# Kernel optimization log

Hardware: AMD Instinct MI355X
Metric: run time of the kernel (lower is better)

The kernel has to match this reference:

```python
import jax, jax.numpy as jnp
import numpy as np

EPS = 1e-5

def conv(x, w, b, stride, pad):
    y = jax.lax.conv_general_dilated(x, w, (stride, stride), [(pad, pad), (pad, pad)],
                                     dimension_numbers=('NCHW', 'OIHW', 'NCHW'))
    return y + b[None, :, None, None]

def inorm(x):
    # InstanceNorm2d, affine=False, eps=1e-5, biased variance over H,W
    m = x.mean(axis=(2, 3), keepdims=True)
    v = ((x - m) ** 2).mean(axis=(2, 3), keepdims=True)
    return (x - m) * jax.lax.rsqrt(v + EPS)

def setup_inputs() -> dict:
    key = jax.random.key(0)
    ks = jax.random.split(key, 24)
    B = 64
    x = jax.random.normal(ks[0], (B, 5, 256, 192), dtype=jnp.float32)
    chans = [(5, 8), (8, 16), (16, 32), (32, 64), (64, 128), (128, 256)]
    params = {'x': x}
    for i, (ci, co) in enumerate(chans):
        fan = ci * 16
        params[f'w{i}'] = jax.random.normal(ks[1 + 2 * i], (co, ci, 4, 4), jnp.float32) / np.sqrt(fan)
        params[f'b{i}'] = jnp.zeros((co,), jnp.float32)
    for i in (6, 7):
        params[f'w{i}'] = jax.random.normal(ks[1 + 2 * i], (256, 256, 3, 3), jnp.float32) / np.sqrt(256 * 9)
        params[f'b{i}'] = jnp.zeros((256,), jnp.float32)
    params['fc1_w'] = jax.random.normal(ks[20], (128, 512), jnp.float32) / np.sqrt(512)
    params['fc1_b'] = jnp.zeros((128,), jnp.float32)
    # fc2: weight zeroed at init in original; use small random for a nontrivial baseline
    params['fc2_w'] = jax.random.normal(ks[21], (50, 128), jnp.float32) * 0.01
    lin = np.linspace(-0.9, 0.9, 5, dtype=np.float32)
    yy, xx = np.meshgrid(lin, lin, indexing='ij')
    tcp = np.stack([xx.ravel(), yy.ravel()], axis=1)  # [25,2]
    params['fc2_b'] = jnp.asarray(np.arctanh(tcp).reshape(-1))  # [50]
    return params

def reference(x, w0, b0, w1, b1, w2, b2, w3, b3, w4, b4, w5, b5, w6, b6, w7, b7,
              fc1_w, fc1_b, fc2_w, fc2_b):
    B = x.shape[0]
    # block 0: conv -> relu -> instance_norm
    h = inorm(jax.nn.relu(conv(x, w0, b0, 2, 1)))
    # blocks 1..5: conv -> instance_norm -> relu, stride 2
    for w, b in ((w1, b1), (w2, b2), (w3, b3), (w4, b4), (w5, b5)):
        h = jax.nn.relu(inorm(conv(h, w, b, 2, 1)))
    # two 3x3 stride-1 blocks
    for w, b in ((w6, b6), (w7, b7)):
        h = jax.nn.relu(inorm(conv(h, w, b, 1, 1)))
    # maxpool 2x2 stride 2
    h = jax.lax.reduce_window(h, -jnp.inf, jax.lax.max, (1, 1, 2, 2), (1, 1, 2, 2), 'VALID')
    h = h.reshape(B, -1)  # [B,512]
    h = jax.nn.relu(h @ fc1_w.T + fc1_b)
    # F.dropout in eval mode = identity (reference is deterministic)
    pts = jnp.tanh(h @ fc2_w.T + fc2_b)  # [B,50]
    coor = pts.reshape(B, -1, 2)          # [B,25,2]
    grid = coor.reshape(B, 5, 5, 2)       # [B, row j, col i, (x,y)]

    # get_row: squared diffs along i, then abs second difference; stack order (j outer, i inner)
    d_row = (grid[:, :, 1:] - grid[:, :, :-1]) ** 2            # [B,5,4,2]
    row = jnp.abs(d_row[:, :, 1:] - d_row[:, :, :-1]).reshape(B, 15, 2)
    # get_col: same along j; stack order (i outer, j inner)
    gT = jnp.swapaxes(grid, 1, 2)                              # [B, i, j, 2]
    d_col = (gT[:, :, 1:] - gT[:, :, :-1]) ** 2
    col = jnp.abs(d_col[:, :, 1:] - d_col[:, :, :-1]).reshape(B, 15, 2)

    # grad_row / grad_col: curvature cross-product terms, BATCH ELEMENT 0 ONLY (as in original)
    def curv(g):  # g: [5,5,2], triplets along axis 1
        p0, p1, p2 = g[:, :-2], g[:, 1:-1], g[:, 2:]
        x0, y0 = p0[..., 0], p0[..., 1]
        x1, y1 = p1[..., 0], p1[..., 1]
        x2, y2 = p2[..., 0], p2[..., 1]
        return jnp.abs((y1 - y0) * (x1 - x2) - (y1 - y2) * (x1 - x0))  # [5,3]

    g0 = grid[0]
    rg_loss = jnp.maximum(curv(g0).sum(), 0.02)
    cg_loss = jnp.maximum(curv(jnp.swapaxes(g0, 0, 1)).sum(), 0.02)

    rx_loss = jnp.maximum(0.08, row[:, :, 0]).mean()
    ry_loss = jnp.maximum(0.08, row[:, :, 1]).mean()
    cx_loss = jnp.maximum(0.08, col[:, :, 0]).mean()
    cy_loss = jnp.maximum(0.08, col[:, :, 1]).mean()
    return (coor, rx_loss, ry_loss, cx_loss, cy_loss, rg_loss, cg_loss)
```

## Files before the change

### kernel.cpp

```cpp
#include <hip/hip_runtime.h>
#include <hip/hip_bf16.h>
#include <math.h>

#define EPS 1e-5f

template<int CIN, int COUT, int H, int W, int TPB>
__global__ __launch_bounds__(TPB) void conv42V(const float* __restrict__ in,
                                               const float* __restrict__ w,
                                               const float* __restrict__ bias,
                                               float* __restrict__ out, int relu)
{
    constexpr int OH  = H / 2, OW = W / 2;
    constexpr int NPX = OH * OW;
    constexpr int PXB = (NPX / 2) / TPB;
    constexpr int NCG = COUT / 8;

    __shared__ float sW[CIN * 8 * 16];
    __shared__ float sB[8];

    int t   = threadIdx.x;
    int bx  = blockIdx.x;
    int pxb = bx % PXB;
    int cg  = (bx / PXB) % NCG;
    int n   = bx / (PXB * NCG);

    for (int i = t; i < CIN * 128; i += TPB) {
        int ci = i >> 7;
        int r  = i & 127;
        int co = r >> 4;
        int k  = r & 15;
        sW[i] = w[((size_t)(cg * 8 + co) * CIN + ci) * 16 + k];
    }
    if (t < 8) sB[t] = bias[cg * 8 + t];
    __syncthreads();

    int px0 = (pxb * TPB + t) * 2;
    int oh  = px0 / OW;
    int ow0 = px0 % OW;
    int ih0 = oh * 2 - 1;
    int iwq = ow0 * 2;

    float acc[8][2];
#pragma unroll
    for (int j = 0; j < 8; ++j) { acc[j][0] = sB[j]; acc[j][1] = sB[j]; }

    const float* ib = in + (size_t)n * CIN * H * W;
#pragma unroll 1
    for (int ci = 0; ci < CIN; ++ci) {
        const float* plane = ib + (size_t)ci * H * W;
#pragma unroll
        for (int kh = 0; kh < 4; ++kh) {
            int ih = ih0 + kh;
            float p[6];
            if ((unsigned)ih < (unsigned)H) {
                const float* row = plane + (size_t)ih * W;
// ... 84 lines not shown
                acc[j][0] = fmaf(p[0], wv.x, acc[j][0]);
                acc[j][0] = fmaf(p[1], wv.y, acc[j][0]);
                acc[j][0] = fmaf(p[2], wv.z, acc[j][0]);
                acc[j][0] = fmaf(p[3], wv.w, acc[j][0]);
                acc[j][1] = fmaf(p[2], wv.x, acc[j][1]);
                acc[j][1] = fmaf(p[3], wv.y, acc[j][1]);
                acc[j][1] = fmaf(p[4], wv.z, acc[j][1]);
                acc[j][1] = fmaf(p[5], wv.w, acc[j][1]);
            }
        }
    }
    float* ob = out + (size_t)n * 8 * 12288 + px0;
#pragma unroll
    for (int j = 0; j < 8; ++j) {
        float2 v;
        v.x = fmaxf(acc[j][0], 0.f);
        v.y = fmaxf(acc[j][1], 0.f);
        *(float2*)(ob + (size_t)j * 12288) = v;
    }
}

__global__ __launch_bounds__(256) void inorm_wave_T768(const float* __restrict__ src,
                                                       float* __restrict__ dst_t)
{
    int gid  = blockIdx.x * blockDim.x + threadIdx.x;
    int wv   = gid >> 6;
    int lane = gid & 63;
    int n = wv >> 5;
    int c = wv & 31;
    const float* p = src + (size_t)wv * 768;
    float tv[12];
    float s1 = 0.f, s2 = 0.f;
#pragma unroll
    for (int k = 0; k < 12; ++k) {
        float v = p[lane + k * 64];
        tv[k] = v;
        s1 += v; s2 += v * v;
    }
    for (int m = 32; m >= 1; m >>= 1) {
        s1 += __shfl_xor(s1, m);
        s2 += __shfl_xor(s2, m);
    }
    float mean = s1 * (1.f / 768.f);
    float var  = s2 * (1.f / 768.f) - mean * mean;
    float r = rsqrtf(var + EPS);
#pragma unroll
    for (int k = 0; k < 12; ++k) {
        int i = lane + k * 64;
        float y = fmaxf((tv[k] - mean) * r, 0.f);
        dst_t[((size_t)c * 768 + i) * 64 + n] = y;
    }
}

__global__ __launch_bounds__(256) void conv_l3t(const float* __restrict__ in_t,
                                                const float* __restrict__ w,
                                                float* __restrict__ pbuf)
{
    int t    = threadIdx.x;
    int lane = t & 63;
    int gw   = __builtin_amdgcn_readfirstlane(blockIdx.x * 4 + (t >> 6));
    int cog  = gw & 31;
    int cic  = (gw >> 5) & 3;
    int oh   = gw >> 7;
    int cc   = cic * 8;
    int co0  = cog * 2;
    int ih0  = 2 * oh - 1;

    float acc[2][12];
#pragma unroll
    for (int j = 0; j < 2; ++j)
#pragma unroll
        for (int p = 0; p < 12; ++p) acc[j][p] = 0.f;

    const float* wb = w + ((size_t)co0 * 32 + cc) * 16;

#pragma unroll 1
    for (int ci = 0; ci < 8; ++ci) {
        const float* pl = in_t + (size_t)(cc + ci) * 768 * 64 + lane;
        float wr[2][16];
#pragma unroll
        for (int k = 0; k < 16; ++k) {
            wr[0][k] = wb[(0 * 32 + ci) * 16 + k];
            wr[1][k] = wb[(1 * 32 + ci) * 16 + k];
        }
#pragma unroll
        for (int kh = 0; kh < 4; ++kh) {
            int ih = ih0 + kh;
            float p[26];
            p[0] = 0.f; p[25] = 0.f;
            if ((unsigned)ih < 32u) {
#pragma unroll
                for (int c = 0; c < 24; ++c)
                    p[c + 1] = pl[(size_t)(ih * 24 + c) * 64];
            } else {
#pragma unroll
                for (int c = 0; c < 24; ++c) p[c + 1] = 0.f;
            }
#pragma unroll
            for (int ow = 0; ow < 12; ++ow) {
#pragma unroll
                for (int kw = 0; kw < 4; ++kw) {
                    float pv = p[2 * ow + kw];
                    acc[0][ow] = fmaf(pv, wr[0][kh * 4 + kw], acc[0][ow]);
                    acc[1][ow] = fmaf(pv, wr[1][kh * 4 + kw], acc[1][ow]);
                }
            }
        }
    }

    float* pb = pbuf + ((size_t)cic * 4096 + (size_t)lane * 64 + co0) * 192 + oh * 12;
#pragma unroll
    for (int j = 0; j < 2; ++j) {
        float4* o4 = (float4*)(pb + (size_t)j * 192);
        o4[0] = make_float4(acc[j][0], acc[j][1], acc[j][2],  acc[j][3]);
        o4[1] = make_float4(acc[j][4], acc[j][5], acc[j][6],  acc[j][7]);
        o4[2] = make_float4(acc[j][8], acc[j][9], acc[j][10], acc[j][11]);
    }
}

__global__ __launch_bounds__(256) void reduce_norm_l3T(const float* __restrict__ pbuf,
                                                       float* __restrict__ dst_t)
{
    int gid  = blockIdx.x * blockDim.x + threadIdx.x;
    int wv   = gid >> 6;
    int lane = gid & 63;
    int n  = wv >> 6;
    int co = wv & 63;
    float tv[3];
#pragma unroll
    for (int k = 0; k < 3; ++k) {
        int i = lane + k * 64;
        float sum = 0.f;
#pragma unroll
        for (int s = 0; s < 4; ++s)
            sum += pbuf[((size_t)s * 4096 + wv) * 192 + i];
        tv[k] = sum;
    }
    float s1 = tv[0] + tv[1] + tv[2];
    float s2 = tv[0]*tv[0] + tv[1]*tv[1] + tv[2]*tv[2];
    for (int m = 32; m >= 1; m >>= 1) {
        s1 += __shfl_xor(s1, m);
        s2 += __shfl_xor(s2, m);
    }
    float mean = s1 * (1.f / 192.f);
    float var  = s2 * (1.f / 192.f) - mean * mean;
    float r = rsqrtf(var + EPS);
#pragma unroll
    for (int k = 0; k < 3; ++k) {
        int i = lane + k * 64;
        float y = fmaxf((tv[k] - mean) * r, 0.f);
        dst_t[((size_t)co * 192 + i) * 64 + n] = y;
    }
}

template<int TPB, int VPT>
__global__ void inorm_blockv(float* __restrict__ data, int relu)
{
    const int HW = TPB * VPT * 4;
    float4* p = (float4*)(data + (size_t)blockIdx.x * HW);
    float4 v[VPT];
    float s = 0.f, q = 0.f;
#pragma unroll
    for (int k = 0; k < VPT; ++k) {
        v[k] = p[threadIdx.x + k * TPB];
        s += v[k].x + v[k].y + v[k].z + v[k].w;
        q += v[k].x*v[k].x + v[k].y*v[k].y + v[k].z*v[k].z + v[k].w*v[k].w;
    }
    for (int m2 = 32; m2 >= 1; m2 >>= 1) {
        s += __shfl_xor(s, m2);
        q += __shfl_xor(q, m2);
    }
    __shared__ float ss[TPB / 64], sq[TPB / 64], sm[2];
    int wave = threadIdx.x >> 6, lane = threadIdx.x & 63;
    if (lane == 0) { ss[wave] = s; sq[wave] = q; }
    __syncthreads();
    if (threadIdx.x == 0) {
        float a = 0.f, b2 = 0.f;
#pragma unroll
        for (int k = 0; k < TPB / 64; ++k) { a += ss[k]; b2 += sq[k]; }
        float mm = a / (float)HW;
        float vv = b2 / (float)HW - mm * mm;
        sm[0] = mm; sm[1] = rsqrtf(vv + EPS);
    }
    __syncthreads();
    float m = sm[0], r = sm[1];
#pragma unroll
    for (int k = 0; k < VPT; ++k) {
        float4 y;
        y.x = (v[k].x - m) * r; y.y = (v[k].y - m) * r;
        y.z = (v[k].z - m) * r; y.w = (v[k].w - m) * r;
        if (relu) {
            y.x = fmaxf(y.x, 0.f); y.y = fmaxf(y.y, 0.f);
            y.z = fmaxf(y.z, 0.f); y.w = fmaxf(y.w, 0.f);
        }
        p[threadIdx.x + k * TPB] = y;
    }
}

__global__ __launch_bounds__(256) void conv_l4(const float* __restrict__ in_t,
                                               const float* __restrict__ w,
                                               float* __restrict__ pbuf)
{
    int t    = threadIdx.x;
    int lane = t & 63;
    int gw   = __builtin_amdgcn_readfirstlane(blockIdx.x * 4 + (t >> 6));
    int cog  = gw & 63;
    int cic  = (gw >> 6) & 7;
    int half = gw >> 9;
    int cc   = cic * 8;
    int co0  = cog * 2;
    int oh0  = half * 4;

    float acc[2][24];
#pragma unroll
    for (int j = 0; j < 2; ++j)
#pragma unroll
        for (int p = 0; p < 24; ++p) acc[j][p] = 0.f;

    const float* wp = w + ((size_t)co0 * 64 + cc) * 16;

#pragma unroll 1
    for (int ci = 0; ci < 8; ++ci) {
        const float* pl = in_t + (size_t)(cc + ci) * 192 * 64 + lane;
        float wr[2][16];
#pragma unroll
        for (int k = 0; k < 16; ++k) {
            wr[0][k] = wp[(0 * 64 + ci) * 16 + k];
            wr[1][k] = wp[(1 * 64 + ci) * 16 + k];
        }
#pragma unroll
        for (int kh = 0; kh < 4; ++kh) {
            float p[4][12];
#pragma unroll
            for (int o = 0; o < 4; ++o) {
                int ih = 2 * (oh0 + o) - 1 + kh;
                if ((unsigned)ih < 16u) {
#pragma unroll
                    for (int c = 0; c < 12; ++c)
                        p[o][c] = pl[(size_t)(ih * 12 + c) * 64];
                } else {
#pragma unroll
                    for (int c = 0; c < 12; ++c) p[o][c] = 0.f;
                }
            }
#pragma unroll
            for (int o = 0; o < 4; ++o)
#pragma unroll
                for (int ow = 0; ow < 6; ++ow) {
#pragma unroll
                    for (int kw = 0; kw < 4; ++kw) {
                        int iw = 2 * ow - 1 + kw;
                        if (iw < 0 || iw >= 12) continue;
                        float pv = p[o][iw];
                        acc[0][o * 6 + ow] = fmaf(pv, wr[0][kh * 4 + kw], acc[0][o * 6 + ow]);
                        acc[1][o * 6 + ow] = fmaf(pv, wr[1][kh * 4 + kw], acc[1][o * 6 + ow]);
                    }
                }
        }
    }

    float* pb = pbuf + ((size_t)(cic * 64 + lane) * 128 + co0) * 48 + oh0 * 6;
#pragma unroll
    for (int j = 0; j < 2; ++j) {
        float4* o4 = (float4*)(pb + j * 48);
#pragma unroll
        for (int q = 0; q < 6; ++q)
            o4[q] = make_float4(acc[j][q * 4 + 0], acc[j][q * 4 + 1],
                                acc[j][q * 4 + 2], acc[j][q * 4 + 3]);
    }
}

__global__ __launch_bounds__(256) void reduce_norm48(const float* __restrict__ pbuf,
                                                     float* __restrict__ out)
{
    int g  = blockIdx.x * blockDim.x + threadIdx.x;
    int co = g & 127;
    int n  = g >> 7;
    float s[48];
#pragma unroll
    for (int p = 0; p < 48; ++p) s[p] = 0.f;
#pragma unroll 1
    for (int c = 0; c < 8; ++c) {
        const float4* p4 = (const float4*)(pbuf + ((size_t)(c * 64 + n) * 128 + co) * 48);
#pragma unroll
        for (int q = 0; q < 12; ++q) {
            float4 a = p4[q];
            s[q * 4 + 0] += a.x; s[q * 4 + 1] += a.y;
            s[q * 4 + 2] += a.z; s[q * 4 + 3] += a.w;
        }
    }
    float m = 0.f;
#pragma unroll
    for (int p = 0; p < 48; ++p) m += s[p];
    m *= (1.f / 48.f);
    float q = 0.f;
#pragma unroll
    for (int p = 0; p < 48; ++p) { float d = s[p] - m; q += d * d; }
    q *= (1.f / 48.f);
    float r = rsqrtf(q + EPS);
    float4* o4 = (float4*)(out + ((size_t)n * 128 + co) * 48);
#pragma unroll
    for (int qq = 0; qq < 12; ++qq) {
        float4 v;
        v.x = fmaxf((s[qq * 4 + 0] - m) * r, 0.f);
        v.y = fmaxf((s[qq * 4 + 1] - m) * r, 0.f);
        v.z = fmaxf((s[qq * 4 + 2] - m) * r, 0.f);
        v.w = fmaxf((s[qq * 4 + 3] - m) * r, 0.f);
        o4[qq] = v;
    }
}

__global__ __launch_bounds__(256) void conv_l67(const float* __restrict__ in,
                                                const float* __restrict__ w,
                                                float* __restrict__ pbuf)
{
    int t    = threadIdx.x;
    int gw   = __builtin_amdgcn_readfirstlane(blockIdx.x * 4 + (t >> 6));
    int lane = t & 63;
    int cic  = gw >> 6;
    int cog  = gw & 63;
    int cc   = cic * 16;
    int co0  = cog * 4;

    float acc[4][12];
#pragma unroll
    for (int j = 0; j < 4; ++j)
#pragma unroll
        for (int p = 0; p < 12; ++p) acc[j][p] = 0.f;

    const float* ip = in + ((size_t)lane * 256 + cc) * 12;
    const float* wp = w + ((size_t)co0 * 256 + cc) * 9;

#pragma unroll 2
    for (int ci = 0; ci < 16; ++ci) {
        float p[12];
        const float4* p4 = (const float4*)(ip + ci * 12);
        float4 a0 = p4[0], a1 = p4[1], a2 = p4[2];
        p[0] = a0.x; p[1] = a0.y; p[2]  = a0.z; p[3]  = a0.w;
        p[4] = a1.x; p[5] = a1.y; p[6]  = a1.z; p[7]  = a1.w;
        p[8] = a2.x; p[9] = a2.y; p[10] = a2.z; p[11] = a2.w;
#pragma unroll
        for (int j = 0; j < 4; ++j) {
            const float* wj = wp + ((size_t)j * 256 + ci) * 9;
            float wr[9];
#pragma unroll
            for (int k = 0; k < 9; ++k) wr[k] = wj[k];
#pragma unroll
            for (int oh = 0; oh < 4; ++oh)
#pragma unroll
                for (int ow = 0; ow < 3; ++ow)
#pragma unroll
                    for (int kh = 0; kh < 3; ++kh) {
                        int ih = oh - 1 + kh;
                        if (ih < 0 || ih >= 4) continue;
#pragma unroll
                        for (int kw = 0; kw < 3; ++kw) {
                            int iw = ow - 1 + kw;
                            if (iw < 0 || iw >= 3) continue;
                            acc[j][oh * 3 + ow] =
                                fmaf(p[ih * 3 + iw], wr[kh * 3 + kw], acc[j][oh * 3 + ow]);
                        }
                    }
        }
    }

    float* pb = pbuf + ((size_t)(cic * 64 + lane) * 256 + co0) * 12;
#pragma unroll
    for (int j = 0; j < 4; ++j) {
        float4* o4 = (float4*)(pb + j * 12);
        o4[0] = make_float4(acc[j][0], acc[j][1], acc[j][2],  acc[j][3]);
        o4[1] = make_float4(acc[j][4], acc[j][5], acc[j][6],  acc[j][7]);
        o4[2] = make_float4(acc[j][8], acc[j][9], acc[j][10], acc[j][11]);
    }
}

__global__ __launch_bounds__(256) void conv_l5(const float* __restrict__ in,
                                               const float* __restrict__ w,
                                               float* __restrict__ pbuf)
{
    int t    = threadIdx.x;
    int gw   = __builtin_amdgcn_readfirstlane(blockIdx.x * 4 + (t >> 6));
    int lane = t & 63;
    int cic  = gw >> 6;
    int cog  = gw & 63;
    int cc   = cic * 8;
    int co0  = cog * 4;

    float acc[4][12];
#pragma unroll
    for (int j = 0; j < 4; ++j)
#pragma unroll
        for (int p = 0; p < 12; ++p) acc[j][p] = 0.f;

    const float* ip = in + ((size_t)lane * 128 + cc) * 48;
    const float* wp = w + ((size_t)co0 * 128 + cc) * 16;

#pragma unroll 1
    for (int ci = 0; ci < 8; ++ci) {
        float p[48];
        const float4* p4 = (const float4*)(ip + ci * 48);
#pragma unroll
        for (int q = 0; q < 12; ++q) {
            float4 a = p4[q];
            p[q * 4 + 0] = a.x; p[q * 4 + 1] = a.y; p[q * 4 + 2] = a.z; p[q * 4 + 3] = a.w;
        }
#pragma unroll
        for (int j = 0; j < 4; ++j) {
            const float* wj = wp + ((size_t)j * 128 + ci) * 16;
            float wr[16];
#pragma unroll
            for (int k = 0; k < 16; ++k) wr[k] = wj[k];
#pragma unroll
            for (int oh = 0; oh < 4; ++oh)
#pragma unroll
                for (int ow = 0; ow < 3; ++ow) {
                    int ih0 = 2 * oh - 1, iw0 = 2 * ow - 1;
#pragma unroll
                    for (int kh = 0; kh < 4; ++kh) {
                        int ih = ih0 + kh;
                        if (ih < 0 || ih >= 8) continue;
#pragma unroll
                        for (int kw = 0; kw < 4; ++kw) {
                            int iw = iw0 + kw;
                            if (iw < 0 || iw >= 6) continue;
                            acc[j][oh * 3 + ow] =
                                fmaf(p[ih * 6 + iw], wr[kh * 4 + kw], acc[j][oh * 3 + ow]);
                        }
                    }
                }
        }
    }

    float* pb = pbuf + ((size_t)(cic * 64 + lane) * 256 + co0) * 12;
#pragma unroll
    for (int j = 0; j < 4; ++j) {
        float4* o4 = (float4*)(pb + j * 12);
        o4[0] = make_float4(acc[j][0], acc[j][1], acc[j][2],  acc[j][3]);
        o4[1] = make_float4(acc[j][4], acc[j][5], acc[j][6],  acc[j][7]);
        o4[2] = make_float4(acc[j][8], acc[j][9], acc[j][10], acc[j][11]);
    }
}

__global__ __launch_bounds__(256) void reduce_norm12(const float* __restrict__ pbuf,
                                                     float* __restrict__ out)
{
    int g  = blockIdx.x * blockDim.x + threadIdx.x;
    int co = g & 255;
    int n  = g >> 8;
    float s[12];
#pragma unroll
    for (int p = 0; p < 12; ++p) s[p] = 0.f;
#pragma unroll 1
    for (int c = 0; c < 16; ++c) {
        const float4* p4 = (const float4*)(pbuf + ((size_t)(c * 64 + n) * 256 + co) * 12);
        float4 a = p4[0], b = p4[1], d = p4[2];
        s[0] += a.x; s[1] += a.y; s[2]  += a.z; s[3]  += a.w;
        s[4] += b.x; s[5] += b.y; s[6]  += b.z; s[7]  += b.w;
        s[8] += d.x; s[9] += d.y; s[10] += d.z; s[11] += d.w;
    }
    float m = 0.f;
#pragma unroll
    for (int p = 0; p < 12; ++p) m += s[p];
    m *= (1.f / 12.f);
    float q = 0.f;
#pragma unroll
    for (int p = 0; p < 12; ++p) { float d = s[p] - m; q += d * d; }
    q *= (1.f / 12.f);
    float r = rsqrtf(q + EPS);
    float* op = out + ((size_t)n * 256 + co) * 12;
    float4* o4 = (float4*)op;
    float y[12];
#pragma unroll
    for (int p = 0; p < 12; ++p) y[p] = fmaxf((s[p] - m) * r, 0.f);
    o4[0] = make_float4(y[0], y[1], y[2],  y[3]);
    o4[1] = make_float4(y[4], y[5], y[6],  y[7]);
    o4[2] = make_float4(y[8], y[9], y[10], y[11]);
}

__global__ void pool_kernel(const float* __restrict__ in, float* __restrict__ out)
{
    int idx = blockIdx.x * blockDim.x + threadIdx.x;
    if (idx >= 64 * 512) return;
    int f = idx & 511;
    int n = idx >> 9;
    int c = f >> 1;
    int h = f & 1;
    const float* p = in + (((size_t)n * 256 + c) * 4 + h * 2) * 3;
    out[idx] = fmaxf(fmaxf(p[0], p[1]), fmaxf(p[3], p[4]));
}

__global__ void fc1_kernel(const float* __restrict__ in, const float* __restrict__ w,
                           const float* __restrict__ b, float* __restrict__ out)
{
    int idx = blockIdx.x * blockDim.x + threadIdx.x;
    if (idx >= 64 * 128) return;
    int j = idx & 127;
    int n = idx >> 7;
    const float* x  = in + n * 512;
    const float* wr = w + j * 512;
    float acc = b[j];
    for (int f = 0; f < 512; ++f) acc = fmaf(x[f], wr[f], acc);
    out[idx] = fmaxf(acc, 0.f);
}

__global__ void fc2_kernel(const float* __restrict__ in, const float* __restrict__ w,
                           const float* __restrict__ b, float* __restrict__ out)
{
    int idx = blockIdx.x * blockDim.x + threadIdx.x;
    if (idx >= 64 * 50) return;
    int k = idx % 50;
    int n = idx / 50;
    const float* x  = in + n * 128;
    const float* wr = w + k * 128;
    float acc = b[k];
    for (int f = 0; f < 128; ++f) acc = fmaf(x[f], wr[f], acc);
    out[idx] = tanhf(acc);
}

__global__ void loss_kernel(const float* __restrict__ pts, float* __restrict__ out)
{
    __shared__ float acc[4][64];
    int n = threadIdx.x;
    float rx = 0.f, ry = 0.f, cx = 0.f, cy = 0.f;
    {
        const float* g = pts + n * 50;
        for (int r = 0; r < 5; ++r)
            for (int j = 0; j < 3; ++j)
                for (int d = 0; d < 2; ++d) {
                    float a0 = g[(r * 5 + j) * 2 + d];
                    float a1 = g[(r * 5 + j + 1) * 2 + d];
                    float a2 = g[(r * 5 + j + 2) * 2 + d];
                    float d0 = (a1 - a0) * (a1 - a0);
                    float d1 = (a2 - a1) * (a2 - a1);
                    float t = fmaxf(0.08f, fabsf(d1 - d0));
                    if (d == 0) rx += t; else ry += t;
                }
        for (int r = 0; r < 5; ++r)
            for (int j = 0; j < 3; ++j)
                for (int d = 0; d < 2; ++d) {
                    float a0 = g[(j * 5 + r) * 2 + d];
                    float a1 = g[((j + 1) * 5 + r) * 2 + d];
                    float a2 = g[((j + 2) * 5 + r) * 2 + d];
                    float d0 = (a1 - a0) * (a1 - a0);
                    float d1 = (a2 - a1) * (a2 - a1);
                    float t = fmaxf(0.08f, fabsf(d1 - d0));
                    if (d == 0) cx += t; else cy += t;
                }
    }
    acc[0][n] = rx; acc[1][n] = ry; acc[2][n] = cx; acc[3][n] = cy;
    __syncthreads();
    if (n == 0) {
        float s0 = 0.f, s1 = 0.f, s2 = 0.f, s3 = 0.f;
        for (int i = 0; i < 64; ++i) {
            s0 += acc[0][i]; s1 += acc[1][i]; s2 += acc[2][i]; s3 += acc[3][i];
        }
        float inv = 1.0f / (64.0f * 15.0f);
        out[3200] = s0 * inv;
        out[3201] = s1 * inv;
        out[3202] = s2 * inv;
        out[3203] = s3 * inv;
        const float* g = pts;
        float rg = 0.f, cg = 0.f;
        for (int r = 0; r < 5; ++r)
            for (int j = 0; j < 3; ++j) {
                float x0 = g[(r * 5 + j) * 2],     y0 = g[(r * 5 + j) * 2 + 1];
                float x1 = g[(r * 5 + j + 1) * 2], y1 = g[(r * 5 + j + 1) * 2 + 1];
                float x2 = g[(r * 5 + j + 2) * 2], y2 = g[(r * 5 + j + 2) * 2 + 1];
                rg += fabsf((y1 - y0) * (x1 - x2) - (y1 - y2) * (x1 - x0));
            }
        for (int r = 0; r < 5; ++r)
            for (int j = 0; j < 3; ++j) {
                float x0 = g[(j * 5 + r) * 2],       y0 = g[(j * 5 + r) * 2 + 1];
                float x1 = g[((j + 1) * 5 + r) * 2], y1 = g[((j + 1) * 5 + r) * 2 + 1];
                float x2 = g[((j + 2) * 5 + r) * 2], y2 = g[((j + 2) * 5 + r) * 2 + 1];
                cg += fabsf((y1 - y0) * (x1 - x2) - (y1 - y2) * (x1 - x0));
            }
        out[3204] = fmaxf(rg, 0.02f);
        out[3205] = fmaxf(cg, 0.02f);
    }
}

extern "C" void kernel_launch(void* const* d_in, const int* in_sizes, int n_in,
                              void* d_out, int out_size, void* d_ws, size_t ws_size,
                              hipStream_t stream)
{
    const float* x = (const float*)d_in[0];
    const float* w[8], *bia[8];
    for (int i = 0; i < 6; ++i) { w[i] = (const float*)d_in[1 + 2 * i]; bia[i] = (const float*)d_in[2 + 2 * i]; }
    w[6] = (const float*)d_in[13]; bia[6] = (const float*)d_in[14];
    w[7] = (const float*)d_in[15]; bia[7] = (const float*)d_in[16];
    const float* fc1_w = (const float*)d_in[17];
    const float* fc1_b = (const float*)d_in[18];
    const float* fc2_w = (const float*)d_in[19];
    const float* fc2_b = (const float*)d_in[20];
    float* out = (float*)d_out;

    float* A      = (float*)d_ws;
    float* Bf     = A + 6291456;
    float* pooled = Bf + 3145728;
    float* fc1o   = pooled + 32768;
    float* At2    = A + 1572864;
    float* pbuf3  = A + 3145728;
    float* At     = A;
    float* l4out  = A + 1048576;
    float* pbuf   = A + 3145728;

    const int N = 64;

    conv0<<<1536, 256, 0, stream>>>(x, w[0], bia[0], A);
    inorm_blockv<256, 12><<<N * 8, 256, 0, stream>>>(A, 0);

    conv42V<8, 16, 128, 96, 256><<<768, 256, 0, stream>>>(A, w[1], bia[1], Bf, 0);
    inorm_blockv<256, 3><<<N * 16, 256, 0, stream>>>(Bf, 1);

    conv42V<16, 32, 64, 48, 192><<<512, 192, 0, stream>>>(Bf, w[2], bia[2], A, 0);
    inorm_wave_T768<<<512, 256, 0, stream>>>(A, At2);

    conv_l3t<<<512, 256, 0, stream>>>(At2, w[3], pbuf3);
    reduce_norm_l3T<<<1024, 256, 0, stream>>>(pbuf3, At);

    conv_l4<<<256, 256, 0, stream>>>(At, w[4], pbuf);
    reduce_norm48<<<32, 256, 0, stream>>>(pbuf, l4out);

    conv_l5<<<256, 256, 0, stream>>>(l4out, w[5], pbuf);
    reduce_norm12<<<64, 256, 0, stream>>>(pbuf, Bf);

    conv_l67<<<256, 256, 0, stream>>>(Bf, w[6], pbuf);
    reduce_norm12<<<64, 256, 0, stream>>>(pbuf, A);

    conv_l67<<<256, 256, 0, stream>>>(A, w[7], pbuf);
    float* l7out = Bf + 262144;
    reduce_norm12<<<64, 256, 0, stream>>>(pbuf, l7out);

    pool_kernel<<<(64 * 512 + 255) / 256, 256, 0, stream>>>(l7out, pooled);
    fc1_kernel<<<(64 * 128 + 255) / 256, 256, 0, stream>>>(pooled, fc1_w, fc1_b, fc1o);
    fc2_kernel<<<(64 * 50 + 255) / 256, 256, 0, stream>>>(fc1o, fc2_w, fc2_b, out);
    loss_kernel<<<1, 64, 0, stream>>>(out, out);
}
```

Measured before the change: 423.3 us.

## Fuse tail layers 3-7 and FC head into one cooperative persistent kernel

Replaces the sequence of conv/reduce/pool/fc/loss launches for layers 3 onward with a single cooperative kernel of 256 blocks. Stages are separated by grid-wide syncs instead of kernel boundaries, so per-launch overhead and tail idle time between small kernels go away. The cost is that each stage now runs on a fixed 256-block grid, with grid-stride loops where more work items existed before, and every stage pays a grid barrier. If the cooperative launch fails, the code falls back to the original separate kernels.

```diff
diff --git a/kernel.cpp b/kernel.cpp
--- a/kernel.cpp
+++ b/kernel.cpp
@@ -1,6 +1,9 @@
 #include <hip/hip_runtime.h>
 #include <hip/hip_bf16.h>
+#include <hip/hip_cooperative_groups.h>
 #include <math.h>
+
+namespace cg = cooperative_groups;
 
 #define EPS 1e-5f
 
@@ -191,107 +194,6 @@
     }
 }
 
-__global__ __launch_bounds__(256) void conv_l3t(const float* __restrict__ in_t,
-                                                const float* __restrict__ w,
-                                                float* __restrict__ pbuf)
-{
-    int t    = threadIdx.x;
-    int lane = t & 63;
-    int gw   = __builtin_amdgcn_readfirstlane(blockIdx.x * 4 + (t >> 6));
-    int cog  = gw & 31;
-    int cic  = (gw >> 5) & 3;
-    int oh   = gw >> 7;
-    int cc   = cic * 8;
-    int co0  = cog * 2;
-    int ih0  = 2 * oh - 1;
-
-    float acc[2][12];
-#pragma unroll
-    for (int j = 0; j < 2; ++j)
-#pragma unroll
-        for (int p = 0; p < 12; ++p) acc[j][p] = 0.f;
-
-    const float* wb = w + ((size_t)co0 * 32 + cc) * 16;
-
-#pragma unroll 1
-    for (int ci = 0; ci < 8; ++ci) {
-        const float* pl = in_t + (size_t)(cc + ci) * 768 * 64 + lane;
-        float wr[2][16];
-#pragma unroll
-        for (int k = 0; k < 16; ++k) {
-            wr[0][k] = wb[(0 * 32 + ci) * 16 + k];
-            wr[1][k] = wb[(1 * 32 + ci) * 16 + k];
-        }
-#pragma unroll
-        for (int kh = 0; kh < 4; ++kh) {
-            int ih = ih0 + kh;
-            float p[26];
-            p[0] = 0.f; p[25] = 0.f;
-            if ((unsigned)ih < 32u) {
-#pragma unroll
-                for (int c = 0; c < 24; ++c)
-                    p[c + 1] = pl[(size_t)(ih * 24 + c) * 64];
-            } else {
-#pragma unroll
-                for (int c = 0; c < 24; ++c) p[c + 1] = 0.f;
-            }
-#pragma unroll
-            for (int ow = 0; ow < 12; ++ow) {
-#pragma unroll
-                for (int kw = 0; kw < 4; ++kw) {
-                    float pv = p[2 * ow + kw];
-                    acc[0][ow] = fmaf(pv, wr[0][kh * 4 + kw], acc[0][ow]);
-                    acc[1][ow] = fmaf(pv, wr[1][kh * 4 + kw], acc[1][ow]);
-                }
-            }
-        }
-    }
-
-    float* pb = pbuf + ((size_t)cic * 4096 + (size_t)lane * 64 + co0) * 192 + oh * 12;
-#pragma unroll
-    for (int j = 0; j < 2; ++j) {
-        float4* o4 = (float4*)(pb + (size_t)j * 192);
-        o4[0] = make_float4(acc[j][0], acc[j][1], acc[j][2],  acc[j][3]);
-        o4[1] = make_float4(acc[j][4], acc[j][5], acc[j][6],  acc[j][7]);
-        o4[2] = make_float4(acc[j][8], acc[j][9], acc[j][10], acc[j][11]);
-    }
-}
-
-__global__ __launch_bounds__(256) void reduce_norm_l3T(const float* __restrict__ pbuf,
-                                                       float* __restrict__ dst_t)
-{
-    int gid  = blockIdx.x * blockDim.x + threadIdx.x;
-    int wv   = gid >> 6;
-    int lane = gid & 63;
-    int n  = wv >> 6;
-    int co = wv & 63;
-    float tv[3];
-#pragma unroll
-    for (int k = 0; k < 3; ++k) {
-        int i = lane + k * 64;
-        float sum = 0.f;
-#pragma unroll
-        for (int s = 0; s < 4; ++s)
-            sum += pbuf[((size_t)s * 4096 + wv) * 192 + i];
-        tv[k] = sum;
-    }
-    float s1 = tv[0] + tv[1] + tv[2];
-    float s2 = tv[0]*tv[0] + tv[1]*tv[1] + tv[2]*tv[2];
-    for (int m = 32; m >= 1; m >>= 1) {
-        s1 += __shfl_xor(s1, m);
-        s2 += __shfl_xor(s2, m);
-    }
-    float mean = s1 * (1.f / 192.f);
-    float var  = s2 * (1.f / 192.f) - mean * mean;
-    float r = rsqrtf(var + EPS);
-#pragma unroll
-    for (int k = 0; k < 3; ++k) {
-        int i = lane + k * 64;
-        float y = fmaxf((tv[k] - mean) * r, 0.f);
-        dst_t[((size_t)co * 192 + i) * 64 + n] = y;
-    }
-}
-
 template<int TPB, int VPT>
 __global__ void inorm_blockv(float* __restrict__ data, int relu)
 {
@@ -336,16 +238,111 @@
     }
 }
 
-__global__ __launch_bounds__(256) void conv_l4(const float* __restrict__ in_t,
-                                               const float* __restrict__ w,
-                                               float* __restrict__ pbuf)
-{
-    int t    = threadIdx.x;
-    int lane = t & 63;
-    int gw   = __builtin_amdgcn_readfirstlane(blockIdx.x * 4 + (t >> 6));
-    int cog  = gw & 63;
-    int cic  = (gw >> 6) & 7;
-    int half = gw >> 9;
+
+__device__ __forceinline__ void l3conv_body(const float* __restrict__ At2,
+                                            const float* __restrict__ w3,
+                                            float* __restrict__ pbuf,
+                                            int wid, int lane)
+{
+    int cog = wid & 31;
+    int cic = (wid >> 5) & 3;
+    int oh  = wid >> 7;
+    int cc  = cic * 8;
+    int co0 = cog * 2;
+    int ih0 = 2 * oh - 1;
+
+    float acc[2][12];
+#pragma unroll
+    for (int j = 0; j < 2; ++j)
+#pragma unroll
+        for (int p = 0; p < 12; ++p) acc[j][p] = 0.f;
+
+    const float* wb = w3 + ((size_t)co0 * 32 + cc) * 16;
+
+#pragma unroll 1
+    for (int ci = 0; ci < 8; ++ci) {
+        const float* pl = At2 + (size_t)(cc + ci) * 768 * 64 + lane;
+        float wr[2][16];
+#pragma unroll
+        for (int k = 0; k < 16; ++k) {
+            wr[0][k] = wb[(0 * 32 + ci) * 16 + k];
+            wr[1][k] = wb[(1 * 32 + ci) * 16 + k];
+        }
+#pragma unroll
+        for (int kh = 0; kh < 4; ++kh) {
+            int ih = ih0 + kh;
+            float p[26];
+            p[0] = 0.f; p[25] = 0.f;
+            if ((unsigned)ih < 32u) {
+#pragma unroll
+                for (int c = 0; c < 24; ++c)
+                    p[c + 1] = pl[(size_t)(ih * 24 + c) * 64];
+            } else {
+#pragma unroll
+                for (int c = 0; c < 24; ++c) p[c + 1] = 0.f;
+            }
+#pragma unroll
+            for (int ow = 0; ow < 12; ++ow) {
+#pragma unroll
+                for (int kw = 0; kw < 4; ++kw) {
+                    float pv = p[2 * ow + kw];
+                    acc[0][ow] = fmaf(pv, wr[0][kh * 4 + kw], acc[0][ow]);
+                    acc[1][ow] = fmaf(pv, wr[1][kh * 4 + kw], acc[1][ow]);
+                }
+            }
+        }
+    }
+    float* pb = pbuf + ((size_t)cic * 4096 + (size_t)lane * 64 + co0) * 192 + oh * 12;
+#pragma unroll
+    for (int j = 0; j < 2; ++j) {
+        float4* o4 = (float4*)(pb + (size_t)j * 192);
+        o4[0] = make_float4(acc[j][0], acc[j][1], acc[j][2],  acc[j][3]);
+        o4[1] = make_float4(acc[j][4], acc[j][5], acc[j][6],  acc[j][7]);
+        o4[2] = make_float4(acc[j][8], acc[j][9], acc[j][10], acc[j][11]);
+    }
+}
+
+__device__ __forceinline__ void l3red_body(const float* __restrict__ pbuf,
+                                           float* __restrict__ At,
+                                           int wv, int lane)
+{
+    int n  = wv >> 6;
+    int co = wv & 63;
+    float tv[3];
+#pragma unroll
+    for (int k = 0; k < 3; ++k) {
+        int i = lane + k * 64;
+        float sum = 0.f;
+#pragma unroll
+        for (int s = 0; s < 4; ++s)
+            sum += pbuf[((size_t)s * 4096 + wv) * 192 + i];
+        tv[k] = sum;
+    }
+    float s1 = tv[0] + tv[1] + tv[2];
+    float s2 = tv[0]*tv[0] + tv[1]*tv[1] + tv[2]*tv[2];
+    for (int m = 32; m >= 1; m >>= 1) {
+        s1 += __shfl_xor(s1, m);
+        s2 += __shfl_xor(s2, m);
+    }
+    float mean = s1 * (1.f / 192.f);
+    float var  = s2 * (1.f / 192.f) - mean * mean;
+    float r = rsqrtf(var + EPS);
+#pragma unroll
+    for (int k = 0; k < 3; ++k) {
+        int i = lane + k * 64;
+        float y = fmaxf((tv[k] - mean) * r, 0.f);
+        At[((size_t)co * 192 + i) * 64 + n] = y;
+    }
+}
+
+__device__ __forceinline__ void l4conv_body(const float* __restrict__ At,
+                                            const float* __restrict__ w4,
+                                            float* __restrict__ pbuf,
+                                            int wid, int lane)
+{
+    int cog  = wid & 63;
+    int cic  = (wid >> 6) & 7;
+    int half = wid >> 9;
     int cc   = cic * 8;
     int co0  = cog * 2;
     int oh0  = half * 4;
@@ -356,11 +353,11 @@
 #pragma unroll
         for (int p = 0; p < 24; ++p) acc[j][p] = 0.f;
 
-    const float* wp = w + ((size_t)co0 * 64 + cc) * 16;
+    const float* wp = w4 + ((size_t)co0 * 64 + cc) * 16;
 
 #pragma unroll 1
     for (int ci = 0; ci < 8; ++ci) {
-        const float* pl = in_t + (size_t)(cc + ci) * 192 * 64 + lane;
+        const float* pl = At + (size_t)(cc + ci) * 192 * 64 + lane;
         float wr[2][16];
 #pragma unroll
         for (int k = 0; k < 16; ++k) {
@@ -397,7 +394,6 @@
                 }
         }
     }
-
     float* pb = pbuf + ((size_t)(cic * 64 + lane) * 128 + co0) * 48 + oh0 * 6;
 #pragma unroll
     for (int j = 0; j < 2; ++j) {
@@ -409,10 +405,9 @@
     }
 }
 
-__global__ __launch_bounds__(256) void reduce_norm48(const float* __restrict__ pbuf,
-                                                     float* __restrict__ out)
-{
-    int g  = blockIdx.x * blockDim.x + threadIdx.x;
+__device__ __forceinline__ void red48_body(const float* __restrict__ pbuf,
+                                           float* __restrict__ outp, int g)
+{
     int co = g & 127;
     int n  = g >> 7;
     float s[48];
@@ -437,7 +432,7 @@
     for (int p = 0; p < 48; ++p) { float d = s[p] - m; q += d * d; }
     q *= (1.f / 48.f);
     float r = rsqrtf(q + EPS);
-    float4* o4 = (float4*)(out + ((size_t)n * 128 + co) * 48);
+    float4* o4 = (float4*)(outp + ((size_t)n * 128 + co) * 48);
 #pragma unroll
     for (int qq = 0; qq < 12; ++qq) {
         float4 v;
@@ -449,17 +444,114 @@
     }
 }
 
-__global__ __launch_bounds__(256) void conv_l67(const float* __restrict__ in,
-                                                const float* __restrict__ w,
-                                                float* __restrict__ pbuf)
-{
-    int t    = threadIdx.x;
-    int gw   = __builtin_amdgcn_readfirstlane(blockIdx.x * 4 + (t >> 6));
-    int lane = t & 63;
-    int cic  = gw >> 6;
-    int cog  = gw & 63;
-    int cc   = cic * 16;
-    int co0  = cog * 4;
+__device__ __forceinline__ void l5conv_body(const float* __restrict__ l4out,
+                                            const float* __restrict__ w5,
+                                            float* __restrict__ pbuf,
+                                            int wid, int lane)
+{
+    int cic = wid >> 6;
+    int cog = wid & 63;
+    int cc  = cic * 8;
+    int co0 = cog * 4;
+
+    float acc[4][12];
+#pragma unroll
+    for (int j = 0; j < 4; ++j)
+#pragma unroll
+        for (int p = 0; p < 12; ++p) acc[j][p] = 0.f;
+
+    const float* ip = l4out + ((size_t)lane * 128 + cc) * 48;
+    const float* wp = w5 + ((size_t)co0 * 128 + cc) * 16;
+
+#pragma unroll 1
+    for (int ci = 0; ci < 8; ++ci) {
+        float p[48];
+        const float4* p4 = (const float4*)(ip + ci * 48);
+#pragma unroll
+        for (int q = 0; q < 12; ++q) {
+            float4 a = p4[q];
+            p[q * 4 + 0] = a.x; p[q * 4 + 1] = a.y;
+            p[q * 4 + 2] = a.z; p[q * 4 + 3] = a.w;
+        }
+#pragma unroll
+        for (int j = 0; j < 4; ++j) {
+            const float* wj = wp + ((size_t)j * 128 + ci) * 16;
+            float wr[16];
+#pragma unroll
+            for (int k = 0; k < 16; ++k) wr[k] = wj[k];
+#pragma unroll
+            for (int oh = 0; oh < 4; ++oh)
+#pragma unroll
+                for (int ow = 0; ow < 3; ++ow) {
+                    int ih0 = 2 * oh - 1, iw0 = 2 * ow - 1;
+#pragma unroll
+                    for (int kh = 0; kh < 4; ++kh) {
+                        int ih = ih0 + kh;
+                        if (ih < 0 || ih >= 8) continue;
+#pragma unroll
+                        for (int kw = 0; kw < 4; ++kw) {
+                            int iw = iw0 + kw;
+                            if (iw < 0 || iw >= 6) continue;
+                            acc[j][oh * 3 + ow] =
+                                fmaf(p[ih * 6 + iw], wr[kh * 4 + kw], acc[j][oh * 3 + ow]);
+                        }
+                    }
+                }
+        }
+    }
+    float* pb = pbuf + ((size_t)(cic * 64 + lane) * 256 + co0) * 12;
+#pragma unroll
+    for (int j = 0; j < 4; ++j) {
+        float4* o4 = (float4*)(pb + j * 12);
+        o4[0] = make_float4(acc[j][0], acc[j][1], acc[j][2],  acc[j][3]);
+        o4[1] = make_float4(acc[j][4], acc[j][5], acc[j][6],  acc[j][7]);
+        o4[2] = make_float4(acc[j][8], acc[j][9], acc[j][10], acc[j][11]);
+    }
+}
+
+__device__ __forceinline__ void red12_body(const float* __restrict__ pbuf,
+                                           float* __restrict__ outp, int g)
+{
+    int co = g & 255;
+    int n  = g >> 8;
+    float s[12];
+#pragma unroll
+    for (int p = 0; p < 12; ++p) s[p] = 0.f;
+#pragma unroll 1
+    for (int c = 0; c < 16; ++c) {
+        const float4* p4 = (const float4*)(pbuf + ((size_t)(c * 64 + n) * 256 + co) * 12);
+        float4 a = p4[0], b = p4[1], d = p4[2];
+        s[0] += a.x; s[1] += a.y; s[2]  += a.z; s[3]  += a.w;
+        s[4] += b.x; s[5] += b.y; s[6]  += b.z; s[7]  += b.w;
+        s[8] += d.x; s[9] += d.y; s[10] += d.z; s[11] += d.w;
+    }
+    float m = 0.f;
+#pragma unroll
+    for (int p = 0; p < 12; ++p) m += s[p];
+    m *= (1.f / 12.f);
+    float q = 0.f;
+#pragma unroll
+    for (int p = 0; p < 12; ++p) { float d = s[p] - m; q += d * d; }
+    q *= (1.f / 12.f);
+    float r = rsqrtf(q + EPS);
+    float4* o4 = (float4*)(outp + ((size_t)n * 256 + co) * 12);
+    float y[12];
+#pragma unroll
+    for (int p = 0; p < 12; ++p) y[p] = fmaxf((s[p] - m) * r, 0.f);
+    o4[0] = make_float4(y[0], y[1], y[2],  y[3]);
+    o4[1] = make_float4(y[4], y[5], y[6],  y[7]);
+    o4[2] = make_float4(y[8], y[9], y[10], y[11]);
+}
+
+__device__ __forceinline__ void conv67_body(const float* __restrict__ in,
+                                            const float* __restrict__ w,
+                                            float* __restrict__ pbuf,
+                                            int gw, int lane)
+{
+    int cic = gw >> 6;
+    int cog = gw & 63;
+    int cc  = cic * 16;
+    int co0 = cog * 4;
 
     float acc[4][12];
 #pragma unroll
@@ -502,7 +594,6 @@
                     }
         }
     }
-
     float* pb = pbuf + ((size_t)(cic * 64 + lane) * 256 + co0) * 12;
 #pragma unroll
     for (int j = 0; j < 4; ++j) {
@@ -513,109 +604,200 @@
     }
 }
 
-__global__ __launch_bounds__(256) void conv_l5(const float* __restrict__ in,
-                                               const float* __restrict__ w,
-                                               float* __restrict__ pbuf)
-{
-    int t    = threadIdx.x;
-    int gw   = __builtin_amdgcn_readfirstlane(blockIdx.x * 4 + (t >> 6));
-    int lane = t & 63;
-    int cic  = gw >> 6;
-    int cog  = gw & 63;
-    int cc   = cic * 8;
-    int co0  = cog * 4;
-
-    float acc[4][12];
-#pragma unroll
-    for (int j = 0; j < 4; ++j)
-#pragma unroll
-        for (int p = 0; p < 12; ++p) acc[j][p] = 0.f;
-
-    const float* ip = in + ((size_t)lane * 128 + cc) * 48;
-    const float* wp = w + ((size_t)co0 * 128 + cc) * 16;
+__global__ __launch_bounds__(256) void coop_tail(const float* __restrict__ w3,
+                                                 const float* __restrict__ w4,
+                                                 const float* __restrict__ w5,
+                                                 const float* __restrict__ w6,
+                                                 const float* __restrict__ w7,
+                                                 const float* __restrict__ fc1_w,
+                                                 const float* __restrict__ fc1_b,
+                                                 const float* __restrict__ fc2_w,
+                                                 const float* __restrict__ fc2_b,
+                                                 float* __restrict__ out,
+                                                 float* __restrict__ ws)
+{
+    cg::grid_group grid = cg::this_grid();
+    __shared__ float smem[3520];
+
+    float* At    = ws;
+    float* At2   = ws + 1572864;
+    float* l4out = ws + 1048576;
+    float* pbuf  = ws + 3145728;
+    float* Bf    = ws + 6291456;
+    float* l7out = Bf + 262144;
+    float* fc1o  = ws + 9469952;
+
+    int t      = threadIdx.x;
+    int lane   = t & 63;
+    int waveId = __builtin_amdgcn_readfirstlane(blockIdx.x * 4 + (t >> 6));
+    int g      = blockIdx.x * 256 + t;
 
 #pragma unroll 1
-    for (int ci = 0; ci < 8; ++ci) {
-        float p[48];
-        const float4* p4 = (const float4*)(ip + ci * 48);
-#pragma unroll
-        for (int q = 0; q < 12; ++q) {
-            float4 a = p4[q];
-            p[q * 4 + 0] = a.x; p[q * 4 + 1] = a.y; p[q * 4 + 2] = a.z; p[q * 4 + 3] = a.w;
-        }
-#pragma unroll
-        for (int j = 0; j < 4; ++j) {
-            const float* wj = wp + ((size_t)j * 128 + ci) * 16;
-            float wr[16];
-#pragma unroll
-            for (int k = 0; k < 16; ++k) wr[k] = wj[k];
-#pragma unroll
-            for (int oh = 0; oh < 4; ++oh)
-#pragma unroll
-                for (int ow = 0; ow < 3; ++ow) {
-                    int ih0 = 2 * oh - 1, iw0 = 2 * ow - 1;
-#pragma unroll
-                    for (int kh = 0; kh < 4; ++kh) {
-                        int ih = ih0 + kh;
-                        if (ih < 0 || ih >= 8) continue;
-#pragma unroll
-                        for (int kw = 0; kw < 4; ++kw) {
-                            int iw = iw0 + kw;
-                            if (iw < 0 || iw >= 6) continue;
-                            acc[j][oh * 3 + ow] =
-                                fmaf(p[ih * 6 + iw], wr[kh * 4 + kw], acc[j][oh * 3 + ow]);
-                        }
+    for (int u = 0; u < 2; ++u) l3conv_body(At2, w3, pbuf, waveId + u * 1024, lane);
+    grid.sync();
+
+#pragma unroll 1
+    for (int u = 0; u < 4; ++u) l3red_body(pbuf, At, waveId + u * 1024, lane);
+    grid.sync();
+
+    l4conv_body(At, w4, pbuf, waveId, lane);
+    grid.sync();
+    if (g < 8192) red48_body(pbuf, l4out, g);
+    grid.sync();
+
+    l5conv_body(l4out, w5, pbuf, waveId, lane);
+    grid.sync();
+    if (g < 16384) red12_body(pbuf, Bf, g);
+    grid.sync();
+
+    conv67_body(Bf, w6, pbuf, waveId, lane);
+    grid.sync();
+    if (g < 16384) red12_body(pbuf, At, g);
+    grid.sync();
+
+    conv67_body(At, w7, pbuf, waveId, lane);
+    grid.sync();
+    if (g < 16384) red12_body(pbuf, l7out, g);
+    grid.sync();
+
+    if (blockIdx.x < 32) {
+        int half = t >> 7;
+        int tl   = t & 127;
+        int n    = blockIdx.x * 2 + half;
+        float* sPool = smem + half * 512;
+        for (int f = tl; f < 512; f += 128) {
+            int c = f >> 1;
+            int h = f & 1;
+            const float* p = l7out + (((size_t)n * 256 + c) * 4 + h * 2) * 3;
+            sPool[f] = fmaxf(fmaxf(p[0], p[1]), fmaxf(p[3], p[4]));
+        }
+        __syncthreads();
+        int j = tl;
+        const float* wr = fc1_w + j * 512;
+        float acc = fc1_b[j];
+#pragma unroll 4
+        for (int f = 0; f < 512; ++f) acc = fmaf(sPool[f], wr[f], acc);
+        fc1o[n * 128 + j] = fmaxf(acc, 0.f);
+    }
+    grid.sync();
+
+    if (blockIdx.x == 0) {
+        float* sPts = smem;
+        float* sAcc = smem + 3200;
+        for (int idx = t; idx < 3200; idx += 256) {
+            int n = idx / 50;
+            int k = idx % 50;
+            const float* xv = fc1o + n * 128;
+            const float* wr = fc2_w + k * 128;
+            float acc = fc2_b[k];
+#pragma unroll 4
+            for (int f = 0; f < 128; ++f) acc = fmaf(xv[f], wr[f], acc);
+            float v = tanhf(acc);
+            out[idx]  = v;
+            sPts[idx] = v;
+        }
+        __syncthreads();
+        if (t < 64) {
+            int n = t;
+            float rx = 0.f, ry = 0.f, cx = 0.f, cy = 0.f;
+            const float* gp = sPts + n * 50;
+            for (int r = 0; r < 5; ++r)
+                for (int j = 0; j < 3; ++j)
+                    for (int d = 0; d < 2; ++d) {
+                        float a0 = gp[(r * 5 + j) * 2 + d];
+                        float a1 = gp[(r * 5 + j + 1) * 2 + d];
+                        float a2 = gp[(r * 5 + j + 2) * 2 + d];
+                        float d0 = (a1 - a0) * (a1 - a0);
+                        float d1 = (a2 - a1) * (a2 - a1);
+                        float tt = fmaxf(0.08f, fabsf(d1 - d0));
+                        if (d == 0) rx += tt; else ry += tt;
                     }
+            for (int r = 0; r < 5; ++r)
+                for (int j = 0; j < 3; ++j)
+                    for (int d = 0; d < 2; ++d) {
+                        float a0 = gp[(j * 5 + r) * 2 + d];
+                        float a1 = gp[((j + 1) * 5 + r) * 2 + d];
+                        float a2 = gp[((j + 2) * 5 + r) * 2 + d];
+                        float d0 = (a1 - a0) * (a1 - a0);
+                        float d1 = (a2 - a1) * (a2 - a1);
+                        float tt = fmaxf(0.08f, fabsf(d1 - d0));
+                        if (d == 0) cx += tt; else cy += tt;
+                    }
+            sAcc[0 * 64 + n] = rx; sAcc[1 * 64 + n] = ry;
+            sAcc[2 * 64 + n] = cx; sAcc[3 * 64 + n] = cy;
+        }
+        __syncthreads();
+        if (t == 0) {
+            float s0 = 0.f, s1 = 0.f, s2 = 0.f, s3 = 0.f;
+            for (int i = 0; i < 64; ++i) {
+                s0 += sAcc[0 * 64 + i]; s1 += sAcc[1 * 64 + i];
+                s2 += sAcc[2 * 64 + i]; s3 += sAcc[3 * 64 + i];
+            }
+            float inv = 1.0f / (64.0f * 15.0f);
+            out[3200] = s0 * inv;
+            out[3201] = s1 * inv;
+            out[3202] = s2 * inv;
+            out[3203] = s3 * inv;
+            const float* gp = sPts;
+            float rg = 0.f, cgs = 0.f;
+            for (int r = 0; r < 5; ++r)
+                for (int j = 0; j < 3; ++j) {
+                    float x0 = gp[(r * 5 + j) * 2],     y0 = gp[(r * 5 + j) * 2 + 1];
+                    float x1 = gp[(r * 5 + j + 1) * 2], y1 = gp[(r * 5 + j + 1) * 2 + 1];
+                    float x2 = gp[(r * 5 + j + 2) * 2], y2 = gp[(r * 5 + j + 2) * 2 + 1];
+                    rg += fabsf((y1 - y0) * (x1 - x2) - (y1 - y2) * (x1 - x0));
                 }
-        }
-    }
-
-    float* pb = pbuf + ((size_t)(cic * 64 + lane) * 256 + co0) * 12;
-#pragma unroll
-    for (int j = 0; j < 4; ++j) {
-        float4* o4 = (float4*)(pb + j * 12);
-        o4[0] = make_float4(acc[j][0], acc[j][1], acc[j][2],  acc[j][3]);
-        o4[1] = make_float4(acc[j][4], acc[j][5], acc[j][6],  acc[j][7]);
-        o4[2] = make_float4(acc[j][8], acc[j][9], acc[j][10], acc[j][11]);
-    }
-}
-
-__global__ __launch_bounds__(256) void reduce_norm12(const float* __restrict__ pbuf,
-                                                     float* __restrict__ out)
-{
-    int g  = blockIdx.x * blockDim.x + threadIdx.x;
-    int co = g & 255;
-    int n  = g >> 8;
-    float s[12];
-#pragma unroll
-    for (int p = 0; p < 12; ++p) s[p] = 0.f;
-#pragma unroll 1
-    for (int c = 0; c < 16; ++c) {
-        const float4* p4 = (const float4*)(pbuf + ((size_t)(c * 64 + n) * 256 + co) * 12);
-        float4 a = p4[0], b = p4[1], d = p4[2];
-        s[0] += a.x; s[1] += a.y; s[2]  += a.z; s[3]  += a.w;
-        s[4] += b.x; s[5] += b.y; s[6]  += b.z; s[7]  += b.w;
-        s[8] += d.x; s[9] += d.y; s[10] += d.z; s[11] += d.w;
-    }
-    float m = 0.f;
-#pragma unroll
-    for (int p = 0; p < 12; ++p) m += s[p];
-    m *= (1.f / 12.f);
-    float q = 0.f;
-#pragma unroll
-    for (int p = 0; p < 12; ++p) { float d = s[p] - m; q += d * d; }
-    q *= (1.f / 12.f);
-    float r = rsqrtf(q + EPS);
-    float* op = out + ((size_t)n * 256 + co) * 12;
-    float4* o4 = (float4*)op;
-    float y[12];
-#pragma unroll
-    for (int p = 0; p < 12; ++p) y[p] = fmaxf((s[p] - m) * r, 0.f);
-    o4[0] = make_float4(y[0], y[1], y[2],  y[3]);
-    o4[1] = make_float4(y[4], y[5], y[6],  y[7]);
-    o4[2] = make_float4(y[8], y[9], y[10], y[11]);
-}
-
+            for (int r = 0; r < 5; ++r)
+                for (int j = 0; j < 3; ++j) {
+                    float x0 = gp[(j * 5 + r) * 2],       y0 = gp[(j * 5 + r) * 2 + 1];
+                    float x1 = gp[((j + 1) * 5 + r) * 2], y1 = gp[((j + 1) * 5 + r) * 2 + 1];
+                    float x2 = gp[((j + 2) * 5 + r) * 2], y2 = gp[((j + 2) * 5 + r) * 2 + 1];
+                    cgs += fabsf((y1 - y0) * (x1 - x2) - (y1 - y2) * (x1 - x0));
+                }
+            out[3204] = fmaxf(rg, 0.02f);
+            out[3205] = fmaxf(cgs, 0.02f);
+        }
+    }
+}
+
+__global__ __launch_bounds__(256) void k_l3conv(const float* At2, const float* w3, float* pbuf)
+{
+    int t = threadIdx.x;
+    l3conv_body(At2, w3, pbuf,
+                __builtin_amdgcn_readfirstlane(blockIdx.x * 4 + (t >> 6)), t & 63);
+}
+__global__ __launch_bounds__(256) void k_l3red(const float* pbuf, float* At)
+{
+    int t = threadIdx.x;
+    l3red_body(pbuf, At,
+               __builtin_amdgcn_readfirstlane(blockIdx.x * 4 + (t >> 6)), t & 63);
+}
+__global__ __launch_bounds__(256) void k_l4conv(const float* At, const float* w4, float* pbuf)
+{
+    int t = threadIdx.x;
+    l4conv_body(At, w4, pbuf,
+                __builtin_amdgcn_readfirstlane(blockIdx.x * 4 + (t >> 6)), t & 63);
+}
+__global__ __launch_bounds__(256) void k_red48(const float* pbuf, float* outp)
+{
+    red48_body(pbuf, outp, blockIdx.x * 256 + threadIdx.x);
+}
+__global__ __launch_bounds__(256) void k_l5conv(const float* in, const float* w5, float* pbuf)
+{
+    int t = threadIdx.x;
+    l5conv_body(in, w5, pbuf,
+                __builtin_amdgcn_readfirstlane(blockIdx.x * 4 + (t >> 6)), t & 63);
+}
+__global__ __launch_bounds__(256) void k_red12(const float* pbuf, float* outp)
+{
+    red12_body(pbuf, outp, blockIdx.x * 256 + threadIdx.x);
+}
+__global__ __launch_bounds__(256) void k_conv67(const float* in, const float* w, float* pbuf)
+{
+    int t = threadIdx.x;
+    conv67_body(in, w, pbuf,
+                __builtin_amdgcn_readfirstlane(blockIdx.x * 4 + (t >> 6)), t & 63);
+}
 __global__ void pool_kernel(const float* __restrict__ in, float* __restrict__ out)
 {
     int idx = blockIdx.x * blockDim.x + threadIdx.x;
@@ -627,7 +809,6 @@
     const float* p = in + (((size_t)n * 256 + c) * 4 + h * 2) * 3;
     out[idx] = fmaxf(fmaxf(p[0], p[1]), fmaxf(p[3], p[4]));
 }
-
 __global__ void fc1_kernel(const float* __restrict__ in, const float* __restrict__ w,
                            const float* __restrict__ b, float* __restrict__ out)
 {
@@ -641,7 +822,6 @@
     for (int f = 0; f < 512; ++f) acc = fmaf(x[f], wr[f], acc);
     out[idx] = fmaxf(acc, 0.f);
 }
-
 __global__ void fc2_kernel(const float* __restrict__ in, const float* __restrict__ w,
                            const float* __restrict__ b, float* __restrict__ out)
 {
@@ -655,7 +835,6 @@
     for (int f = 0; f < 128; ++f) acc = fmaf(x[f], wr[f], acc);
     out[idx] = tanhf(acc);
 }
-
 __global__ void loss_kernel(const float* __restrict__ pts, float* __restrict__ out)
 {
     __shared__ float acc[4][64];
@@ -734,15 +913,14 @@
     const float* fc2_b = (const float*)d_in[20];
     float* out = (float*)d_out;
 
-    float* A      = (float*)d_ws;
-    float* Bf     = A + 6291456;
-    float* pooled = Bf + 3145728;
-    float* fc1o   = pooled + 32768;
-    float* At2    = A + 1572864;
-    float* pbuf3  = A + 3145728;
-    float* At     = A;
-    float* l4out  = A + 1048576;
-    float* pbuf   = A + 3145728;
+    float* A     = (float*)d_ws;
+    float* At    = A;
+    float* At2   = A + 1572864;
+    float* l4out = A + 1048576;
+    float* pbuf  = A + 3145728;
+    float* Bf    = A + 6291456;
+    float* l7out = Bf + 262144;
+    float* fc1o  = A + 9469952;
 
     const int N = 64;
 
@@ -755,24 +933,29 @@
     conv42V<16, 32, 64, 48, 192><<<512, 192, 0, stream>>>(Bf, w[2], bia[2], A, 0);
     inorm_wave_T768<<<512, 256, 0, stream>>>(A, At2);
 
-    conv_l3t<<<512, 256, 0, stream>>>(At2, w[3], pbuf3);
-    reduce_norm_l3T<<<1024, 256, 0, stream>>>(pbuf3, At);
-
-    conv_l4<<<256, 256, 0, stream>>>(At, w[4], pbuf);
-    reduce_norm48<<<32, 256, 0, stream>>>(pbuf, l4out);
-
-    conv_l5<<<256, 256, 0, stream>>>(l4out, w[5], pbuf);
-    reduce_norm12<<<64, 256, 0, stream>>>(pbuf, Bf);
-
-    conv_l67<<<256, 256, 0, stream>>>(Bf, w[6], pbuf);
-    reduce_norm12<<<64, 256, 0, stream>>>(pbuf, A);
-
-    conv_l67<<<256, 256, 0, stream>>>(A, w[7], pbuf);
-    float* l7out = Bf + 262144;
-    reduce_norm12<<<64, 256, 0, stream>>>(pbuf, l7out);
-
-    pool_kernel<<<(64 * 512 + 255) / 256, 256, 0, stream>>>(l7out, pooled);
-    fc1_kernel<<<(64 * 128 + 255) / 256, 256, 0, stream>>>(pooled, fc1_w, fc1_b, fc1o);
-    fc2_kernel<<<(64 * 50 + 255) / 256, 256, 0, stream>>>(fc1o, fc2_w, fc2_b, out);
-    loss_kernel<<<1, 64, 0, stream>>>(out, out);
-}
+    float* ws_f = A;
+    void* args[] = {
+        (void*)&w[3], (void*)&w[4], (void*)&w[5], (void*)&w[6], (void*)&w[7],
+        (void*)&fc1_w, (void*)&fc1_b, (void*)&fc2_w, (void*)&fc2_b,
+        (void*)&out, (void*)&ws_f
+    };
+    hipError_t err = hipLaunchCooperativeKernel((void*)coop_tail, dim3(256), dim3(256),
+                                                args, 0, stream);
+    if (err != hipSuccess) {
+        k_l3conv<<<512, 256, 0, stream>>>(At2, w[3], pbuf);
+        k_l3red<<<1024, 256, 0, stream>>>(pbuf, At);
+        k_l4conv<<<256, 256, 0, stream>>>(At, w[4], pbuf);
+        k_red48<<<32, 256, 0, stream>>>(pbuf, l4out);
+        k_l5conv<<<256, 256, 0, stream>>>(l4out, w[5], pbuf);
+        k_red12<<<64, 256, 0, stream>>>(pbuf, Bf);
+        k_conv67<<<256, 256, 0, stream>>>(Bf, w[6], pbuf);
+        k_red12<<<64, 256, 0, stream>>>(pbuf, At);
+        k_conv67<<<256, 256, 0, stream>>>(At, w[7], pbuf);
+        k_red12<<<64, 256, 0, stream>>>(pbuf, l7out);
+        pool_kernel<<<(64 * 512 + 255) / 256, 256, 0, stream>>>(l7out, Bf + 3145728 - 32768);
+        float* pooled = Bf + 3145728 - 32768;
+        fc1_kernel<<<(64 * 128 + 255) / 256, 256, 0, stream>>>(pooled, fc1_w, fc1_b, fc1o);
+        fc2_kernel<<<(64 * 50 + 255) / 256, 256, 0, stream>>>(fc1o, fc2_w, fc2_b, out);
+        loss_kernel<<<1, 64, 0, stream>>>(out, out);
+    }
+}
```

Result: slower. 880.9 us (+108.1%).
